# Kernel optimization log

Hardware: AMD Instinct MI355X
Metric: run time of the kernel (lower is better)

The kernel has to match this reference:

```python
import jax, jax.numpy as jnp
import numpy as np
from math import factorial, sqrt

# ---------------- irreps utilities ----------------
def parse(s):
    out = []
    for tok in s.split('+'):
        tok = tok.strip()
        mul, ir = (tok.split('x') if 'x' in tok else ('1', tok))
        out.append((int(mul), int(ir[:-1]), 1 if ir[-1] == 'e' else -1))
    return out

def irdim(ir):
    return sum(m * (2 * l + 1) for m, l, p in ir)

def slices(ir):
    s, o = [], 0
    for m, l, p in ir:
        s.append((o, m, l, p)); o += m * (2 * l + 1)
    return s

# ---------------- real Clebsch-Gordan coefficients ----------------
def _cgc(j1, m1, j2, m2, j3, m3):
    if m1 + m2 != m3:
        return 0.0
    f = factorial
    pre = sqrt((2 * j3 + 1) * f(j3 + j1 - j2) * f(j3 - j1 + j2) * f(j1 + j2 - j3) / f(j1 + j2 + j3 + 1))
    pre *= sqrt(f(j3 + m3) * f(j3 - m3) * f(j1 - m1) * f(j1 + m1) * f(j2 - m2) * f(j2 + m2))
    s = 0.0
    for k in range(max(0, j2 - j3 - m1, j1 - j3 + m2), min(j1 + j2 - j3, j1 - m1, j2 + m2) + 1):
        s += (-1) ** k / (f(k) * f(j1 + j2 - j3 - k) * f(j1 - m1 - k) * f(j2 + m2 - k) * f(j3 - j2 + m1 + k) * f(j3 - j1 - m2 + k))
    return pre * s

def _c2r(l):
    # complex -> real spherical-harmonic change of basis
    q = np.zeros((2 * l + 1, 2 * l + 1), dtype=complex); r2 = 1 / np.sqrt(2)
    q[l, l] = 1.0
    for mu in range(1, l + 1):
        q[mu + l, mu + l] = (-1) ** mu * r2; q[mu + l, -mu + l] = r2
        q[-mu + l, -mu + l] = 1j * r2;       q[-mu + l, mu + l] = -1j * (-1) ** mu * r2
    return q

_CGMEM = {}
def cg_real(l1, l2, l3):
    key = (l1, l2, l3)
    if key in _CGMEM:
        return _CGMEM[key]
    C = np.zeros((2 * l1 + 1, 2 * l2 + 1, 2 * l3 + 1))
    for m1 in range(-l1, l1 + 1):
        for m2 in range(-l2, l2 + 1):
            if abs(m1 + m2) <= l3:
                C[m1 + l1, m2 + l2, m1 + m2 + l3] = _cgc(l1, m1, l2, m2, l3, m1 + m2)
    T = np.einsum('am,bn,co,mno->abc', _c2r(l1), _c2r(l2), np.conj(_c2r(l3)), C)
    R = T.real if np.abs(T.real).sum() >= np.abs(T.imag).sum() else T.imag
    _CGMEM[key] = np.ascontiguousarray(R)
    return _CGMEM[key]

# ---------------- equivariant ops ----------------
def tp_paths(ir1, ir2, iro):
    P = []
    for (o1, m1, l1, p1) in slices(ir1):
        for (o2, m2, l2, p2) in slices(ir2):
            for (oo, mo, lo, po) in slices(iro):
                if po == p1 * p2 and abs(l1 - l2) <= lo <= l1 + l2:
                    P.append((o1, m1, l1, o2, m2, l2, oo, mo, lo))
    return P

def tp_numel(P):
    return sum(m1 * m2 * mo for (_, m1, _, _, m2, _, _, mo, _) in P)

def tp_apply(ir1, ir2, iro, x1, x2, w):
    # FullyConnectedTensorProduct with per-row (shared_weights=False) weights w:[E, numel]
    P = tp_paths(ir1, ir2, iro)
    out = jnp.zeros((x1.shape[0], irdim(iro)), x1.dtype)
    fan = {}
    for p in P:
        fan[p[6]] = fan.get(p[6], 0) + p[1] * p[4]
    off = 0
    for (o1, m1, l1, o2, m2, l2, oo, mo, lo) in P:
        cg = jnp.asarray(cg_real(l1, l2, lo), x1.dtype)
        a = x1[:, o1:o1 + m1 * (2 * l1 + 1)].reshape(-1, m1, 2 * l1 + 1)
        b = x2[:, o2:o2 + m2 * (2 * l2 + 1)].reshape(-1, m2, 2 * l2 + 1)
        ww = w[:, off:off + m1 * m2 * mo].reshape(-1, m1, m2, mo); off += m1 * m2 * mo
        r = jnp.einsum('eui,evj,euvw,ijk->ewk', a, b, ww, cg) / np.sqrt(fan[oo])
        out = out.at[:, oo:oo + mo * (2 * lo + 1)].add(r.reshape(-1, mo * (2 * lo + 1)))
    return out

def lin_pairs(iri, iro):
    return [(si, so) for si in slices(iri) for so in slices(iro) if si[2] == so[2] and si[3] == so[3]]

def lin_numel(iri, iro):
    return sum(si[1] * so[1] for si, so in lin_pairs(iri, iro))

def lin_apply(iri, iro, x, w):
    # o3.Linear: per-irrep channel mixing with fan-in normalization
    out = jnp.zeros((x.shape[0], irdim(iro)), x.dtype)
    pairs = lin_pairs(iri, iro)
    fan = {}
    for si, so in pairs:
        fan[so[0]] = fan.get(so[0], 0) + si[1]
    off = 0
    for (oi, mi, li, pi), (oo, mo, lo, po) in pairs:
        W = w[off:off + mi * mo].reshape(mi, mo); off += mi * mo
        xb = x[:, oi:oi + mi * (2 * li + 1)].reshape(-1, mi, 2 * li + 1)
        r = jnp.einsum('eui,uv->evi', xb, W) / np.sqrt(fan[oo])
        out = out.at[:, oo:oo + mo * (2 * lo + 1)].add(r.reshape(-1, mo * (2 * lo + 1)))
    return out

def act_apply(ir, acts, x):
    # tanh on scalar irreps only (flags in acts), identity elsewhere
    parts = []
    for (o, m, l, p), a in zip(slices(ir), acts):
        b = x[:, o:o + m * (2 * l + 1)]
        parts.append(jnp.tanh(b) if a else b)
    return jnp.concatenate(parts, axis=1)

def fc_apply(x, w, dims):
    # e3nn FullyConnectedNet: relu MLP with 1/sqrt(fan_in) weight normalization
    off, h = 0, x
    for i in range(len(dims) - 1):
        di, do = dims[i], dims[i + 1]
        W = w[off:off + di * do].reshape(di, do); off += di * do
        h = (h @ W) / np.sqrt(di)
        if i < len(dims) - 2:
            h = jax.nn.relu(h)
    return h

# ---------------- module irreps (from V_theta.__init__) ----------------
IRR_IN = parse('2x0e')
IRR_SH = parse('1x0e+1x1o+1x2e')
MID1 = parse('8x0e+8x1o+8x2e')
MID2 = parse('8x0e+8x0o+8x1e+8x1o+8x2e+8x2o')
IRR_HH = parse('4x0e+2x1o+2x1o+1x0e+1x1e+1x2e')
IRR_CC = parse('9x0e+6x1o+3x2e+6x1o+' + '1x0e+1x1e+1x2e+' * 4 + '1x1o+1x2o+1x3o+' * 2 + '3x2e+' + '1x1o+1x2o+1x3o+' * 2 + '1x0e+1x1e+1x2e+1x3e+1x4e')
IRR_CH = parse('6x0e+3x1o+4x1o+' + '1x0e+1x1e+1x2e+' * 2 + '2x2e+1x1o+1x2o+1x3o')
SCR = parse('32x0e+1x2e'); SCR2 = parse('1x0e+1x2e'); G1 = parse('32x0e'); G2 = parse('3x0e')
ACT2 = [1, 0, 0]; ACT3 = [1, 1, 0, 0, 0, 0]
P1 = tp_paths(IRR_IN, IRR_SH, MID1); P2 = tp_paths(MID1, IRR_SH, MID2); PB = tp_paths(MID2, MID2, MID2)
EMB_N = 16
FC1D = [1, EMB_N, EMB_N, EMB_N, tp_numel(P1)]
FC2D = [1, EMB_N, EMB_N, EMB_N, tp_numel(P2)]
FCBD = [1, EMB_N, EMB_N, EMB_N, tp_numel(PB)]

def fcsz(d):
    return sum(d[i] * d[i + 1] for i in range(len(d) - 1))

N_NODES, N_EDGES, N_BOND, SCALING = 10000, 100000, 1000, 0.2


def setup_inputs() -> dict:
    key = jax.random.key(0)
    ks = jax.random.split(key, 32)
    nrm = lambda i, shp: jax.random.normal(ks[i], shp, jnp.float32)
    return {
        'f_in': nrm(0, (N_NODES, 2)),
        'sh': nrm(1, (N_EDGES, 9)),
        'emb': jax.random.uniform(ks[2], (N_EDGES, 1), jnp.float32),
        'num_neighbors': jnp.full((1,), 10.0, jnp.float32),
        'w_lin1': nrm(3, (lin_numel(IRR_IN, IRR_IN),)),
        'w_lin2': nrm(4, (lin_numel(MID1, MID1),)),
        'w_lin3': nrm(5, (lin_numel(MID2, MID2),)),
        'w_linCC': nrm(6, (lin_numel(MID2, IRR_CC),)),
        'w_linHH': nrm(7, (lin_numel(MID2, IRR_HH),)),
        'w_linCH': nrm(8, (lin_numel(MID2, IRR_CH),)),
        'w_linC': nrm(9, (lin_numel(MID2, IRR_CC),)),
        'w_linH': nrm(10, (lin_numel(MID2, IRR_HH),)),
        'w_screen1': nrm(11, (lin_numel(MID2, SCR),)),
        'w_screen2': nrm(12, (lin_numel(SCR, SCR2),)),
        'w_gap1': nrm(13, (lin_numel(MID2, G1),)),
        'w_gap2': nrm(14, (lin_numel(G1, G2),)),
        'w_fc1': nrm(15, (fcsz(FC1D),)),
        'w_fc2': nrm(16, (fcsz(FC2D),)),
        'w_fcb': nrm(17, (fcsz(FCBD),)),
        'edge_src': jax.random.randint(ks[18], (N_EDGES,), 0, N_NODES),
        'edge_dst': jax.random.randint(ks[19], (N_EDGES,), 0, N_NODES),
        'HH_ind': jax.random.randint(ks[20], (N_BOND,), 0, N_EDGES),
        'CC_ind': jax.random.randint(ks[21], (N_BOND,), 0, N_EDGES),
        'CH_ind': jax.random.randint(ks[22], (N_BOND,), 0, N_EDGES),
        'num_nodes': N_NODES,
    }


def reference(f_in, sh, emb, num_neighbors, w_lin1, w_lin2, w_lin3, w_linCC, w_linHH, w_linCH, w_linC, w_linH, w_screen1, w_screen2, w_gap1, w_gap2, w_fc1, w_fc2, w_fcb, edge_src, edge_dst, HH_ind, CC_ind, CH_ind, num_nodes):
    inv = 1.0 / jnp.sqrt(num_neighbors)  # .div(num_neighbors**0.5)
    # layer 1: linear + tanh, gather -> TP with per-edge weights -> scatter-add
    x = jnp.tanh(lin_apply(IRR_IN, IRR_IN, f_in, w_lin1))
    ef = tp_apply(IRR_IN, IRR_SH, MID1, x[edge_src], sh, fc_apply(emb, w_fc1, FC1D))
    x = jax.ops.segment_sum(ef, edge_dst, num_segments=num_nodes) * inv
    x = act_apply(MID1, ACT2, lin_apply(MID1, MID1, x, w_lin2))
    # layer 2
    ef = tp_apply(MID1, IRR_SH, MID2, x[edge_src], sh, fc_apply(emb, w_fc2, FC2D))
    x = jax.ops.segment_sum(ef, edge_dst, num_segments=num_nodes) * inv
    x = act_apply(MID2, ACT3, lin_apply(MID2, MID2, x, w_lin3))
    # bond-level tensor products on edge subsets
    def bond(ind):
        return tp_apply(MID2, MID2, MID2, x[edge_src[ind]], x[edge_dst[ind]], fc_apply(emb[ind], w_fcb, FCBD))
    HHf, CCf, CHf = bond(HH_ind), bond(CC_ind), bond(CH_ind)
    eHH = lin_apply(MID2, IRR_HH, act_apply(MID2, ACT3, HHf), w_linHH)
    eCC = lin_apply(MID2, IRR_CC, act_apply(MID2, ACT3, CCf), w_linCC)
    eCH = lin_apply(MID2, IRR_CH, act_apply(MID2, ACT3, CHf), w_linCH)
    nC = lin_apply(MID2, IRR_CC, x, w_linC)
    nH = lin_apply(MID2, IRR_HH, x, w_linH)
    screen = lin_apply(SCR, SCR2, act_apply(SCR, [1, 0], lin_apply(MID2, SCR, x, w_screen1)), w_screen2)
    def gap(F):
        return lin_apply(G1, G2, jnp.tanh(lin_apply(MID2, G1, F, w_gap1)), w_gap2)
    s = SCALING
    # order: H, C, HH, CH, CC, screen, gap[CC], gap[HH], gap[CH]
    return (nH * s, nC * s, eHH * s, eCH * s, eCC * s, screen, gap(CCf), gap(HHf), gap(CHf))
```

## Files before the change

kernel.cpp:

```cpp
#include <hip/hip_runtime.h>
#include <hip/hip_bf16.h>

typedef __hip_bfloat16 bf16_t;

#define N_NODES 10000
#define N_EDGES 100000
#define N_BONDS 1000

__device__ __forceinline__ float bf2f(bf16_t v){ return __bfloat162float(v); }
__device__ __forceinline__ bf16_t f2bf(float v){ return __float2bfloat16(v); }
__device__ __forceinline__ int iabs(int x){ return x<0?-x:x; }

constexpr bool cg_nz(int l1,int l2,int l3,int i,int j,int k){
  int m1=i-l1, m2=j-l2, m3=k-l3;
  int neg=(m1<0)+(m2<0)+(m3<0);
  if (((neg ^ (l1+l2+l3)) & 1)!=0) return false;
  int a1=m1<0?-m1:m1, a2=m2<0?-m2:m2, a3=m3<0?-m3:m3;
  return (a3==a1+a2)||(a3==a1-a2)||(a3==a2-a1);
}

__device__ __forceinline__ void stout(void* out, size_t idx, float v, bool f32o){
  if (f32o) ((float*)out)[idx]=v;
  else      ((bf16_t*)out)[idx]=f2bf(v);
}

__global__ void detect_k(const unsigned short* nnb_raw, int* flag){
  *flag = (nnb_raw[0]==0x4120) ? 0 : 1;
}

struct CvtArgs {
  const void* src[19];
  float* dst[19];
  int n[19];
};

__global__ __launch_bounds__(256) void convert_k(CvtArgs a, const int* flag){
  bool f32 = (*flag)!=0;
  int tid = blockIdx.x*256+threadIdx.x;
  int nth = gridDim.x*256;
  for(int t=0;t<19;++t){
    int n=a.n[t];
    float* d=a.dst[t];
    if (f32){
      const float* s=(const float*)a.src[t];
      for(int i=tid;i<n;i+=nth) d[i]=s[i];
    } else {
      const bf16_t* s=(const bf16_t*)a.src[t];
      for(int i=tid;i<n;i+=nth) d[i]=bf2f(s[i]);
    }
  }
}

__global__ __launch_bounds__(256) void csr_count_k(const int* __restrict__ edst, int* __restrict__ cnt){
  int e=blockIdx.x*256+threadIdx.x; if(e>=N_EDGES) return;
  atomicAdd(&cnt[edst[e]],1);
}

__global__ __launch_bounds__(256) void csr_scan_k(const int* __restrict__ cnt,
    int* __restrict__ rowptr, int* __restrict__ pos){
  __shared__ int ssum[256];
  int t=threadIdx.x;
  int base=t*40;
  int s=0;
  for(int i=0;i<40;++i){ int idx=base+i; s += (idx<N_NODES)? cnt[idx]:0; }
  ssum[t]=s; __syncthreads();
  if(t==0){ int run=0; for(int i=0;i<256;++i){ int v=ssum[i]; ssum[i]=run; run+=v; } }
  __syncthreads();
  int run=ssum[t];
  for(int i=0;i<40;++i){
    int idx=base+i;
    if(idx<N_NODES){ rowptr[idx]=run; pos[idx]=run; run+=cnt[idx]; }
  }
  if(t==255) rowptr[N_NODES]=run;
}

__global__ __launch_bounds__(256) void csr_scatter_k(const int* __restrict__ edst,
    int* __restrict__ pos, int* __restrict__ sorted){
  int e=blockIdx.x*256+threadIdx.x; if(e>=N_EDGES) return;
  int p=atomicAdd(&pos[edst[e]],1);
  sorted[p]=e;
}

__device__ __forceinline__ double dfact(int n){
  const double F[11]={1.,1.,2.,6.,24.,120.,720.,5040.,40320.,362880.,3628800.};
  return F[n];
}

__device__ double cgc_d(int j1,int m1,int j2,int m2,int j3,int m3){
  if (m1+m2!=m3) return 0.0;
  double pre = sqrt((double)(2*j3+1)*dfact(j3+j1-j2)*dfact(j3-j1+j2)*dfact(j1+j2-j3)/dfact(j1+j2+j3+1));
  pre *= sqrt(dfact(j3+m3)*dfact(j3-m3)*dfact(j1-m1)*dfact(j1+m1)*dfact(j2-m2)*dfact(j2+m2));
  int k0 = max(0, max(j2-j3-m1, j1-j3+m2));
  int k1 = min(j1+j2-j3, min(j1-m1, j2+m2));
  double s=0.0;
  for(int k=k0;k<=k1;++k)
    s += ((k&1)?-1.0:1.0)/(dfact(k)*dfact(j1+j2-j3-k)*dfact(j1-m1-k)*dfact(j2+m2-k)*dfact(j3-j2+m1+k)*dfact(j3-j1-m2+k));
  return pre*s;
}

__device__ void c2r_d(int l,int a,int m,double&re,double&im){
  re=0.0; im=0.0;
  const double r2 = 0.7071067811865475244;
  int mu = a-l;
  if (mu==0){ if (m==l) re=1.0; return; }
  if (mu>0){
    if (m==l+mu) re = (mu&1)? -r2 : r2;
    else if (m==l-mu) re = r2;
  } else {
    int nu=-mu;
    if (m==l-nu) im = r2;
    else if (m==l+nu) im = (nu&1)? r2 : -r2;
  }
}

__global__ __launch_bounds__(128) void cg_init_k(float* cg){
  int b=blockIdx.x;
  int l1=b/9, l2=(b/3)%3, l3=b%3;
  if (l3 < iabs(l1-l2) || l3 > l1+l2) return;
  int n1=2*l1+1,n2=2*l2+1,n3=2*l3+1,n=n1*n2*n3;
  __shared__ double sRe[125], sIm[125];
  __shared__ int sPick;
  int t=threadIdx.x;
  if (t<n){
    int a=t/(n2*n3), bb=(t/n3)%n2, c=t%n3;
    double re=0.0, im=0.0;
    for(int m1=0;m1<n1;++m1){
      double q1r,q1i; c2r_d(l1,a,m1,q1r,q1i);
      if (q1r==0.0 && q1i==0.0) continue;
      for(int m2=0;m2<n2;++m2){
        double q2r,q2i; c2r_d(l2,bb,m2,q2r,q2i);
        if (q2r==0.0 && q2i==0.0) continue;
        int m3=(m1-l1)+(m2-l2)+l3;
        if (m3<0||m3>=n3) continue;
        double q3r,q3i; c2r_d(l3,c,m3,q3r,q3i); q3i=-q3i;
        double C = cgc_d(l1,m1-l1,l2,m2-l2,l3,m3-l3);
        if (C==0.0) continue;
        double ar = q1r*q2r - q1i*q2i;
        double ai = q1r*q2i + q1i*q2r;
        re += (ar*q3r - ai*q3i)*C;
        im += (ar*q3i + ai*q3r)*C;
      }
    }
    sRe[t]=re; sIm[t]=im;
  }
  __syncthreads();
  if (t==0){
    double s1=0.0,s2=0.0;
    for(int i=0;i<n;++i){ s1+=fabs(sRe[i]); s2+=fabs(sIm[i]); }
    sPick = (s1>=s2)?1:0;
  }
  __syncthreads();
  if (t<n) cg[b*125+t] = (float)(sPick? sRe[t] : sIm[t]);
}

__global__ __launch_bounds__(256) void nodeA_k(const float* __restrict__ fin,
                                               const float* __restrict__ w,
                                               float* __restrict__ x1){
  int n=blockIdx.x*256+threadIdx.x; if(n>=N_NODES) return;
  float f0=fin[2*n], f1=fin[2*n+1];
  const float r2=0.70710678f;
// ... 160 lines not shown
  float* Xw=sX+ns*72;
  Xw[v]=r[0];
  #pragma unroll
  for(int i=0;i<3;++i) Xw[8+v*3+i]=r[1+i];
  #pragma unroll
  for(int i=0;i<5;++i) Xw[32+v*5+i]=r[4+i];
  __syncthreads();
  for(int t=tid;t<32*72;t+=256){
    int n=base+t/72;
    if (n<N_NODES) x[(size_t)n*72 + t%72]=sX[t];
  }
}

__global__ __launch_bounds__(256) void lin3b_k(float* __restrict__ x, const float* __restrict__ w){
  __shared__ float sX[32*144];
  __shared__ float sW[384];
  int tid=threadIdx.x;
  int base=blockIdx.x*32;
  for(int t=tid;t<384;t+=256) sW[t]=w[t];
  for(int t=tid;t<32*144;t+=256){
    int n=base+t/144;
    sX[t] = (n<N_NODES)? x[(size_t)n*144 + t%144] : 0.f;
  }
  __syncthreads();
  int ns=tid>>3, v=tid&7;
  const float r8=0.35355339f;
  const float* X=sX+ns*144;
  float r[18];
  {
    float a=0.f;
    #pragma unroll
    for(int u=0;u<8;++u) a+=X[u]*sW[u*8+v];
    r[0]=tanhf(a*r8);
  }
  {
    float a=0.f;
    #pragma unroll
    for(int u=0;u<8;++u) a+=X[8+u]*sW[64+u*8+v];
    r[1]=tanhf(a*r8);
  }
  #pragma unroll
  for(int i=0;i<3;++i){
    float a=0.f;
    #pragma unroll
    for(int u=0;u<8;++u) a+=X[16+u*3+i]*sW[128+u*8+v];
    r[2+i]=a*r8;
  }
  #pragma unroll
  for(int i=0;i<3;++i){
    float a=0.f;
    #pragma unroll
    for(int u=0;u<8;++u) a+=X[40+u*3+i]*sW[192+u*8+v];
    r[5+i]=a*r8;
  }
  #pragma unroll
  for(int i=0;i<5;++i){
    float a=0.f;
    #pragma unroll
    for(int u=0;u<8;++u) a+=X[64+u*5+i]*sW[256+u*8+v];
    r[8+i]=a*r8;
  }
  #pragma unroll
  for(int i=0;i<5;++i){
    float a=0.f;
    #pragma unroll
    for(int u=0;u<8;++u) a+=X[104+u*5+i]*sW[320+u*8+v];
    r[13+i]=a*r8;
  }
  __syncthreads();
  float* Xw=sX+ns*144;
  Xw[v]=r[0];
  Xw[8+v]=r[1];
  #pragma unroll
  for(int i=0;i<3;++i) Xw[16+v*3+i]=r[2+i];
  #pragma unroll
  for(int i=0;i<3;++i) Xw[40+v*3+i]=r[5+i];
  #pragma unroll
  for(int i=0;i<5;++i) Xw[64+v*5+i]=r[8+i];
  #pragma unroll
  for(int i=0;i<5;++i) Xw[104+v*5+i]=r[13+i];
  __syncthreads();
  for(int t=tid;t<32*144;t+=256){
    int n=base+t/144;
    if (n<N_NODES) x[(size_t)n*144 + t%144]=sX[t];
  }
}

template<int L1,int L2,int LO,int BO,int SLOT>
__device__ __forceinline__ void tp_acc(const float* Au, const float* b,
    const float* __restrict__ cg, float wv, float* acc){
  constexpr int D1=2*L1+1, D2=2*L2+1, DN=2*LO+1;
  const float* C = cg + ((L1*3+L2)*3+LO)*125;
  float P[DN];
  #pragma unroll
  for(int k=0;k<DN;++k) P[k]=0.f;
  #pragma unroll
  for(int i=0;i<D1;++i){
    float av=Au[i];
    #pragma unroll
    for(int j=0;j<D2;++j){
      #pragma unroll
      for(int k=0;k<DN;++k){
        if (cg_nz(L1,L2,LO,i,j,k)){
          float cv=C[(i*D2+j)*DN+k];
          P[k]+=av*(cv*b[BO+j]);
        }
      }
    }
  }
  #pragma unroll
  for(int k=0;k<DN;++k) acc[SLOT+k]+=wv*P[k];
}

__device__ __forceinline__ void e2_finish2(float* acc, float inv, float* __restrict__ o, bool first){
  int lane=threadIdx.x&63;
  int w=lane&7;
  #pragma unroll
  for(int t=0;t<18;++t){
    acc[t]+=__shfl_xor(acc[t],8,64);
    acc[t]+=__shfl_xor(acc[t],16,64);
    acc[t]+=__shfl_xor(acc[t],32,64);
  }
  if (lane<8){
    float f0 =rsqrtf(24.f)*inv;
    float f1e=rsqrtf(16.f)*inv;
    float f1o=rsqrtf(32.f)*inv;
    float f2e=rsqrtf(32.f)*inv;
    float f2o=rsqrtf(16.f)*inv;
    if (first){
      o[0+w]=acc[0]*f0;
      o[8+w]=0.f;
      #pragma unroll
      for(int k=0;k<3;++k) o[16+w*3+k]=acc[2+k]*f1e;
      #pragma unroll
      for(int k=0;k<3;++k) o[40+w*3+k]=acc[5+k]*f1o;
      #pragma unroll
      for(int k=0;k<5;++k) o[64+w*5+k]=acc[8+k]*f2e;
      #pragma unroll
      for(int k=0;k<5;++k) o[104+w*5+k]=acc[13+k]*f2o;
    } else {
      o[0+w]+=acc[0]*f0;
      #pragma unroll
      for(int k=0;k<3;++k) o[16+w*3+k]+=acc[2+k]*f1e;
      #pragma unroll
      for(int k=0;k<3;++k) o[40+w*3+k]+=acc[5+k]*f1o;
      #pragma unroll
      for(int k=0;k<5;++k) o[64+w*5+k]+=acc[8+k]*f2e;
      #pragma unroll
      for(int k=0;k<5;++k) o[104+w*5+k]+=acc[13+k]*f2o;
    }
  }
}

__device__ __forceinline__ void e2c_consume(const float* __restrict__ xn,
    const float* __restrict__ sh, const float* __restrict__ cg,
    const float* wwp, int e, int src, int u, int lane, float* acc){
  float sv[15];
  sv[ 0]=wwp[  0+lane]; sv[ 1]=wwp[256+lane]; sv[ 2]=wwp[768+lane];
  sv[ 3]=wwp[320+lane]; sv[ 4]=wwp[832+lane];
  sv[ 5]=wwp[ 64+lane]; sv[ 6]=wwp[192+lane]; sv[ 7]=wwp[448+lane]; sv[ 8]=wwp[640+lane];
  sv[ 9]=wwp[128+lane]; sv[10]=wwp[384+lane]; sv[11]=wwp[576+lane]; sv[12]=wwp[896+lane];
  sv[13]=wwp[512+lane]; sv[14]=wwp[704+lane];
  const float* A = xn + (size_t)src*72;
  float b[9];
  #pragma unroll
  for(int j=0;j<9;++j) b[j]=sh[(size_t)e*9+j];
  float a0[1]; a0[0]=A[u];
  float a1[3];
  #pragma unroll
  for(int i=0;i<3;++i) a1[i]=A[8+u*3+i];
  float a2[5];
  #pragma unroll
  for(int i=0;i<5;++i) a2[i]=A[32+u*5+i];
  tp_acc<0,0,0,0, 0>(a0,b,cg,sv[ 0],acc);
  tp_acc<1,1,0,1, 0>(a1,b,cg,sv[ 1],acc);
  tp_acc<2,2,0,4, 0>(a2,b,cg,sv[ 2],acc);
  tp_acc<1,1,1,1, 2>(a1,b,cg,sv[ 3],acc);
  tp_acc<2,2,1,4, 2>(a2,b,cg,sv[ 4],acc);
  tp_acc<0,1,1,1, 5>(a0,b,cg,sv[ 5],acc);
  tp_acc<1,0,1,0, 5>(a1,b,cg,sv[ 6],acc);
  tp_acc<1,2,1,4, 5>(a1,b,cg,sv[ 7],acc);
  tp_acc<2,1,1,1, 5>(a2,b,cg,sv[ 8],acc);
  tp_acc<0,2,2,4, 8>(a0,b,cg,sv[ 9],acc);
  tp_acc<1,1,2,1, 8>(a1,b,cg,sv[10],acc);
  tp_acc<2,0,2,0, 8>(a2,b,cg,sv[11],acc);
  tp_acc<2,2,2,4, 8>(a2,b,cg,sv[12],acc);
  tp_acc<1,2,2,4,13>(a1,b,cg,sv[13],acc);
  tp_acc<2,1,2,1,13>(a2,b,cg,sv[14],acc);
}

__global__ __launch_bounds__(256) void edge2g_k(const float* __restrict__ xn,
    const float* __restrict__ sh, const float* __restrict__ ww2,
    const int* __restrict__ esrc, const int* __restrict__ sorted,
    const int* __restrict__ rowptr, const float* __restrict__ nnb,
    const float* __restrict__ cg, float* __restrict__ xout,
    int rb, int re, int first){
  int wid=threadIdx.x>>6, lane=threadIdx.x&63;
  int n=blockIdx.x*4+wid; if(n>=N_NODES) return;
  int u=lane>>3;
  float inv=rsqrtf(nnb[0]);
  int r0=rowptr[n], r1=rowptr[n+1];
  int lo=max(r0,rb), hi=min(r1,re);
  if (lo>=hi && !first) return;
  float acc[18];
  #pragma unroll
  for(int t=0;t<18;++t) acc[t]=0.f;
  for(int r=lo;r<hi;++r){
    int e=__builtin_amdgcn_readfirstlane(sorted[r]);
    int src=__builtin_amdgcn_readfirstlane(esrc[e]);
    const float* wr = ww2 + (size_t)(r-rb)*960;
    e2c_consume(xn,sh,cg,wr,e,src,u,lane,acc);
  }
  e2_finish2(acc, inv, xout+(size_t)n*144, first!=0);
}

__global__ __launch_bounds__(256) void edge2c_k(const float* __restrict__ xn,
    const float* __restrict__ sh, const float* __restrict__ h2,
    const float* __restrict__ Wg, const int* __restrict__ esrc,
    const int* __restrict__ sorted, const int* __restrict__ rowptr,
    const float* __restrict__ nnb, const float* __restrict__ cg,
    float* __restrict__ xout){
  __shared__ float ww[2][4][960];
  __shared__ int sE[4];
  __shared__ int sCnt[4];
  int tid=threadIdx.x, wid=tid>>6, lane=tid&63;
  int n=blockIdx.x*4+wid;
  int u=lane>>3;
  float inv=rsqrtf(nnb[0]);
  int r0=rowptr[n], r1=rowptr[n+1];
  if (lane==0) sCnt[wid]=r1-r0;
  __syncthreads();
  int mx = max(max(sCnt[0],sCnt[1]),max(sCnt[2],sCnt[3]));
  float acc[18];
  #pragma unroll
  for(int t=0;t<18;++t) acc[t]=0.f;
  int pe=0, psrc=0; bool pact=false;
  for(int t=0;t<mx;++t){
    int r=r0+t;
    bool act=(r<r1);
    int e=0, src=0;
    if (act){
      e=__builtin_amdgcn_readfirstlane(sorted[r]);
      src=__builtin_amdgcn_readfirstlane(esrc[e]);
    }
    if (lane==0) sE[wid]= act? e : -1;
    __syncthreads();
    if (tid<240){
      int e0=max(sE[0],0), e1=max(sE[1],0), e2i=max(sE[2],0), e3=max(sE[3],0);
      const float* h0=h2+(size_t)e0*16;
      const float* h1=h2+(size_t)e1*16;
      const float* hq=h2+(size_t)e2i*16;
      const float* h3=h2+(size_t)e3*16;
      float4 av[4];
      #pragma unroll
      for(int k=0;k<4;++k) av[k]=make_float4(0.f,0.f,0.f,0.f);
      #pragma unroll
      for(int i=0;i<16;++i){
        float hx=h0[i], hy=h1[i], hz=hq[i], hw=h3[i];
        const float* Wr=Wg+i*960;
        #pragma unroll
        for(int k=0;k<4;++k){
          float w=Wr[tid+240*k];
          av[k].x+=hx*w; av[k].y+=hy*w; av[k].z+=hz*w; av[k].w+=hw*w;
        }
      }
      float* wb=&ww[t&1][0][0];
      #pragma unroll
      for(int k=0;k<4;++k){
        int c=tid+240*k;
        wb[c]=av[k].x*0.25f; wb[960+c]=av[k].y*0.25f;
        wb[1920+c]=av[k].z*0.25f; wb[2880+c]=av[k].w*0.25f;
      }
    }
    if (pact){
      const float* wwp=&ww[(t&1)^1][wid][0];
      e2c_consume(xn,sh,cg,wwp,pe,psrc,u,lane,acc);
    }
    pe=e; psrc=src; pact=act;
    __syncthreads();
  }
  if (pact){
    const float* wwp=&ww[(mx-1)&1][wid][0];
    e2c_consume(xn,sh,cg,wwp,pe,psrc,u,lane,acc);
  }
  e2_finish2(acc, inv, xout+(size_t)n*144, true);
}

struct IrS{ short off,m,l,p; };
__device__ const IrS SL_MID2[6]={{0,8,0,1},{8,8,0,-1},{16,8,1,1},{40,8,1,-1},{64,8,2,1},{104,8,2,-1}};
__device__ const IrS SL_HH[6]={{0,4,0,1},{4,2,1,-1},{10,2,1,-1},{16,1,0,1},{17,1,1,1},{20,1,2,1}};
__device__ const IrS SL_CC[34]={{0,9,0,1},{9,6,1,-1},{27,3,2,1},{42,6,1,-1},
 {60,1,0,1},{61,1,1,1},{64,1,2,1},{69,1,0,1},{70,1,1,1},{73,1,2,1},
 {78,1,0,1},{79,1,1,1},{82,1,2,1},{87,1,0,1},{88,1,1,1},{91,1,2,1},
 {96,1,1,-1},{99,1,2,-1},{104,1,3,-1},{111,1,1,-1},{114,1,2,-1},{119,1,3,-1},
 {126,3,2,1},{141,1,1,-1},{144,1,2,-1},{149,1,3,-1},{156,1,1,-1},{159,1,2,-1},{164,1,3,-1},
 {171,1,0,1},{172,1,1,1},{175,1,2,1},{180,1,3,1},{187,1,4,1}};
__device__ const IrS SL_CH[13]={{0,6,0,1},{6,3,1,-1},{15,4,1,-1},{27,1,0,1},{28,1,1,1},{31,1,2,1},
 {36,1,0,1},{37,1,1,1},{40,1,2,1},{45,2,2,1},{55,1,1,-1},{58,1,2,-1},{63,1,3,-1}};

__device__ void lin_out_r(const float* __restrict__ x, bool act16, const float* __restrict__ w,
                          const IrS* so, int no, void* out, size_t base, bool f32o,
                          float scale, int aBeg, int aEnd, bool zf){
  float tx[16];
  bool need_tx = act16 && (aBeg<2);
  if (need_tx){
    #pragma unroll
    for(int i=0;i<16;++i) tx[i]=tanhf(x[i]);
  }
  if (zf){
    for(int bI=0;bI<no;++bI){
      if (so[bI].l>=3){
        int cnt=so[bI].m*(2*so[bI].l+1);
        for(int t=0;t<cnt;++t) stout(out, base+so[bI].off+t, 0.f, f32o);
      }
    }
  }
  int woff=0;
  float f = 0.35355339f*scale;
  for(int a=0;a<6;++a){
    int la=SL_MID2[a].l, pa=SL_MID2[a].p, oa=SL_MID2[a].off;
    int d=2*la+1;
    bool doit = (a>=aBeg && a<aEnd);
    for(int bI=0;bI<no;++bI){
      if (so[bI].l!=la || so[bI].p!=pa) continue;
      int mo=so[bI].m;
      if (doit){
        for(int v=0;v<mo;++v){
          for(int i=0;i<d;++i){
            float acc=0.f;
            for(int u=0;u<8;++u){
              int idx=oa+u*d+i;
              float xv=(act16 && idx<16)? tx[idx] : x[idx];
              acc+=xv*w[woff+u*mo+v];
            }
            stout(out, base+so[bI].off+v*d+i, acc*f, f32o);
          }
        }
      }
      woff+=8*mo;
    }
  }
}

__global__ __launch_bounds__(256) void node_out_k(const float* __restrict__ x,
    const float* __restrict__ wC, const float* __restrict__ wH,
    const float* __restrict__ ws1, const float* __restrict__ ws2,
    void* out, const int* __restrict__ flag){
  int t=blockIdx.x*256+threadIdx.x;
  int n=t>>3, job=t&7;
  if (n>=N_NODES) return;
  bool f32o = (*flag)!=0;
  const float* X = x + (size_t)n*144;
  if (job==0){
    lin_out_r(X,false,wH,SL_HH,6, out, (size_t)n*25, f32o, 0.2f, 0,6, true);
  } else if (job==1){
    const float r8=0.35355339f, r32=0.17677670f;
    float t0[32];
    for(int v=0;v<32;++v){
      float acc=0.f;
      #pragma unroll
      for(int u=0;u<8;++u) acc+=X[u]*ws1[u*32+v];
      t0[v]=tanhf(acc*r8);
    }
    float t2[5];
    #pragma unroll
    for(int i=0;i<5;++i){
      float acc=0.f;
      #pragma unroll
      for(int u=0;u<8;++u) acc+=X[64+u*5+i]*ws1[256+u];
      t2[i]=acc*r8;
    }
    size_t sb = 2501000 + (size_t)n*6;
    float acc=0.f;
    for(int v=0;v<32;++v) acc+=t0[v]*ws2[v];
    stout(out, sb, acc*r32, f32o);
    float w2e=ws2[32];
    #pragma unroll
    for(int i=0;i<5;++i) stout(out, sb+1+i, t2[i]*w2e, f32o);
  } else if (job>=2 && job<=5){
    const int AB[4]={0,2,4,5}, AE[4]={2,4,5,6};
    lin_out_r(X,false,wC,SL_CC,34, out, 250000 + (size_t)n*196, f32o, 0.2f,
              AB[job-2], AE[job-2], job==2);
  }
}

template<int L1,int L2,int LO>
__device__ __forceinline__ void bond_path2(const float* sa,int ao,const float* sb,int bo,
    const float* __restrict__ cg, const float* __restrict__ wwp,
    float invfan, float* sF, int oo, int lane){
  constexpr int D1=2*L1+1, D2=2*L2+1, DN=2*LO+1;
  const float* C = cg + ((L1*3+L2)*3+LO)*125;
  int u=lane>>3, v=lane&7;
  float P[DN];
  #pragma unroll
  for(int k=0;k<DN;++k) P[k]=0.f;
  #pragma unroll
  for(int i=0;i<D1;++i){
    float avv=sa[ao+u*D1+i];
    #pragma unroll
    for(int j=0;j<D2;++j){
      #pragma unroll
      for(int k=0;k<DN;++k){
        if (cg_nz(L1,L2,LO,i,j,k)){
          float cv=C[(i*D2+j)*DN+k];
          P[k]+=(avv*sb[bo+v*D2+j])*cv;
        }
      }
    }
  }
  int v2=u;
  float acc[DN];
  #pragma unroll
  for(int k=0;k<DN;++k) acc[k]=0.f;
  #pragma unroll
  for(int u2=0;u2<8;++u2){
    float ww=wwp[u2*64 + lane];
    int srcl=u2*8+v2;
    #pragma unroll
    for(int k=0;k<DN;++k) acc[k]+=ww*__shfl(P[k],srcl,64);
  }
  #pragma unroll
  for(int k=0;k<DN;++k){
    acc[k]+=__shfl_xor(acc[k],8,64);
    acc[k]+=__shfl_xor(acc[k],16,64);
    acc[k]+=__shfl_xor(acc[k],32,64);
  }
  int w=lane&7;
  if (v2==0){
    #pragma unroll
    for(int k=0;k<DN;++k) sF[oo+w*DN+k]+=acc[k]*invfan;
  }
}

__device__ __forceinline__ void bond_disp(int code, const float* a,int ao,const float* bb,int bo,
    const float* __restrict__ cg, const float* __restrict__ wwp,
    float fv, float* Ff, int oo, int lane){
  switch(code){
    case 0:  bond_path2<0,0,0>(a,ao,bb,bo,cg,wwp,fv,Ff,oo,lane); break;
    case 4:  bond_path2<0,1,1>(a,ao,bb,bo,cg,wwp,fv,Ff,oo,lane); break;
    case 8:  bond_path2<0,2,2>(a,ao,bb,bo,cg,wwp,fv,Ff,oo,lane); break;
    case 10: bond_path2<1,0,1>(a,ao,bb,bo,cg,wwp,fv,Ff,oo,lane); break;
    case 12: bond_path2<1,1,0>(a,ao,bb,bo,cg,wwp,fv,Ff,oo,lane); break;
    case 13: bond_path2<1,1,1>(a,ao,bb,bo,cg,wwp,fv,Ff,oo,lane); break;
    case 14: bond_path2<1,1,2>(a,ao,bb,bo,cg,wwp,fv,Ff,oo,lane); break;
    case 16: bond_path2<1,2,1>(a,ao,bb,bo,cg,wwp,fv,Ff,oo,lane); break;
    case 17: bond_path2<1,2,2>(a,ao,bb,bo,cg,wwp,fv,Ff,oo,lane); break;
    case 20: bond_path2<2,0,2>(a,ao,bb,bo,cg,wwp,fv,Ff,oo,lane); break;
    case 22: bond_path2<2,1,1>(a,ao,bb,bo,cg,wwp,fv,Ff,oo,lane); break;
    case 23: bond_path2<2,1,2>(a,ao,bb,bo,cg,wwp,fv,Ff,oo,lane); break;
    case 24: bond_path2<2,2,0>(a,ao,bb,bo,cg,wwp,fv,Ff,oo,lane); break;
    case 25: bond_path2<2,2,1>(a,ao,bb,bo,cg,wwp,fv,Ff,oo,lane); break;
    case 26: bond_path2<2,2,2>(a,ao,bb,bo,cg,wwp,fv,Ff,oo,lane); break;
  }
}

__global__ __launch_bounds__(256) void bond_tpl_k(const float* __restrict__ xn,
    const float* __restrict__ hb, const float* __restrict__ Wg,
    const int* __restrict__ esrc, const int* __restrict__ edst,
    const int* __restrict__ i0, const int* __restrict__ i1,
    const int* __restrict__ i2, const float* __restrict__ cg,
    float* __restrict__ F0, float* __restrict__ F1, float* __restrict__ F2){
  __shared__ float sA[4][144], sB[4][144], sF[4][144];
  __shared__ float ww[2][2048];
  int tid=threadIdx.x;
  int wid=tid>>6, lane=tid&63;
  int gb=blockIdx.x*4+wid;
  int s=gb/N_BONDS, bi=gb-s*N_BONDS;
  const int* ind=(s==0)?i0:(s==1)?i1:i2;
  float* F=(s==0)?F0:(s==1)?F1:F2;
  int ie=ind[bi];
  int src=esrc[ie], dst=edst[ie];
  for(int t=lane;t<144;t+=64){
    sA[wid][t]=xn[(size_t)src*144+t];
    sB[wid][t]=xn[(size_t)dst*144+t];
    sF[wid][t]=0.f;
  }
  float4 hreg[16];
  {
    size_t hbase=(size_t)blockIdx.x*64;
    #pragma unroll
    for(int i=0;i<16;++i)
      hreg[i]=make_float4(hb[hbase+i],hb[hbase+16+i],hb[hbase+32+i],hb[hbase+48+i]);
  }
  const int SL_L[6]={0,0,1,1,2,2};
  const int SL_P[6]={1,-1,1,-1,1,-1};
  const int SL_O[6]={0,8,16,40,64,104};
  const float fi0=rsqrtf(384.f), fi1=rsqrtf(768.f);
  int pidx=0;
  int pcode=0, pao=0, pbo=0, poo=0; float pfv=0.f;
  for(int s1=0;s1<6;++s1){
    for(int s2=0;s2<6;++s2){
      for(int so=0;so<6;++so){
        int l1=SL_L[s1], l2=SL_L[s2], lo=SL_L[so];
        if (SL_P[so]!=SL_P[s1]*SL_P[s2]) continue;
        if (lo<iabs(l1-l2) || lo>l1+l2) continue;
        {
          const float* Wp = Wg + (size_t)pidx*512;
          float4 a0=make_float4(0.f,0.f,0.f,0.f);
          float4 a1=make_float4(0.f,0.f,0.f,0.f);
          #pragma unroll
          for(int i=0;i<16;++i){
            float w0=Wp[(size_t)i*30720 + tid];
            float w1=Wp[(size_t)i*30720 + tid + 256];
            float4 h=hreg[i];
            a0.x+=h.x*w0; a0.y+=h.y*w0; a0.z+=h.z*w0; a0.w+=h.w*w0;
            a1.x+=h.x*w1; a1.y+=h.y*w1; a1.z+=h.z*w1; a1.w+=h.w*w1;
          }
          float* wb=ww[pidx&1];
          wb[0*512+tid]    =a0.x*0.25f;
          wb[1*512+tid]    =a0.y*0.25f;
          wb[2*512+tid]    =a0.z*0.25f;
          wb[3*512+tid]    =a0.w*0.25f;
          wb[0*512+tid+256]=a1.x*0.25f;
          wb[1*512+tid+256]=a1.y*0.25f;
          wb[2*512+tid+256]=a1.z*0.25f;
          wb[3*512+tid+256]=a1.w*0.25f;
        }
        if (pidx>0){
          const float* wwp = ww[(pidx-1)&1] + wid*512;
          bond_disp(pcode, sA[wid], pao, sB[wid], pbo, cg, wwp, pfv, sF[wid], poo, lane);
        }
        pcode=l1*9+l2*3+lo; pao=SL_O[s1]; pbo=SL_O[s2]; poo=SL_O[so];
        pfv=(lo==0)? fi0 : fi1;
        pidx++;
        __syncthreads();
      }
    }
  }
  {
    const float* wwp = ww[(pidx-1)&1] + wid*512;
    bond_disp(pcode, sA[wid], pao, sB[wid], pbo, cg, wwp, pfv, sF[wid], poo, lane);
  }
  __syncthreads();
  for(int t=lane;t<144;t+=64) F[(size_t)bi*144+t]=sF[wid][t];
}

__global__ __launch_bounds__(256) void bond_out_k(const float* __restrict__ F,
    const float* __restrict__ wlin, int tbl, void* out, size_t baseE,
    const float* __restrict__ wg1, const float* __restrict__ wg2,
    size_t baseG, const int* __restrict__ flag){
  int t=blockIdx.x*256+threadIdx.x;
  int n=t>>3, job=t&7;
  if (n>=N_BONDS) return;
  bool f32o = (*flag)!=0;
  const float* X=F+(size_t)n*144;
  if (job==0){
    const float r8=0.35355339f, r32=0.17677670f;
    float g[32];
    for(int v=0;v<32;++v){
      float acc=0.f;
      #pragma unroll
      for(int u=0;u<8;++u) acc+=X[u]*wg1[u*32+v];
      g[v]=tanhf(acc*r8);
    }
    #pragma unroll
    for(int c=0;c<3;++c){
      float acc=0.f;
      for(int v=0;v<32;++v) acc+=g[v]*wg2[v*3+c];
      stout(out, baseG+(size_t)n*3+c, acc*r32, f32o);
    }
  } else if (job>=2 && job<=5){
    const IrS* so; int no; int dim;
    if(tbl==0){so=SL_HH;no=6;dim=25;}
    else if(tbl==1){so=SL_CC;no=34;dim=196;}
    else {so=SL_CH;no=13;dim=70;}
    const int AB[4]={0,2,4,5}, AE[4]={2,4,5,6};
    lin_out_r(X,true,wlin,so,no,out,baseE+(size_t)n*dim,f32o,0.2f,
              AB[job-2], AE[job-2], job==2);
  }
}

extern "C" void kernel_launch(void* const* d_in, const int* in_sizes, int n_in,
                              void* d_out, int out_size, void* d_ws, size_t ws_size,
                              hipStream_t stream){
  const int* esrc=(const int*)d_in[19];
  const int* edst=(const int*)d_in[20];
  const int* iHH =(const int*)d_in[21];
  const int* iCC =(const int*)d_in[22];
  const int* iCH =(const int*)d_in[23];
  float* ws=(float*)d_ws;
  int* flag=(int*)d_ws;

  size_t off=16;
  auto alloc=[&](size_t n){ size_t o=off; off+=(n+15)&~(size_t)15; return o; };
  size_t o_cg = alloc(27*125);
  size_t o_st[19];
  for(int i=0;i<19;++i) o_st[i]=alloc((size_t)in_sizes[i]);
  size_t o_x1  = alloc(20000);
  size_t o_xM1 = alloc(720000);
  size_t o_xM2 = alloc(1440000);
  size_t o_F0  = alloc(144000);
  size_t o_F1  = alloc(144000);
  size_t o_F2  = alloc(144000);
  size_t o_h1  = alloc((size_t)N_EDGES*16);
  size_t o_h2  = alloc((size_t)N_EDGES*16);
  size_t o_hb  = alloc((size_t)3*N_BONDS*16);
  size_t o_ww1 = alloc((size_t)N_EDGES*48);
  size_t o_cnt = alloc(10016);
  size_t o_rp  = alloc(10016);
  size_t o_pos = alloc(10016);
  size_t o_srt = alloc(N_EDGES);

  float* cg  = ws+o_cg;
  float* x1  = ws+o_x1;
  float* xM1 = ws+o_xM1;
  float* xM2 = ws+o_xM2;
  float* F0  = ws+o_F0;
  float* F1  = ws+o_F1;
  float* F2  = ws+o_F2;
  float* h1  = ws+o_h1;
  float* h2  = ws+o_h2;
  float* hb  = ws+o_hb;
  float* ww1 = ws+o_ww1;
  int* cnt   = (int*)(ws+o_cnt);
  int* rowptr= (int*)(ws+o_rp);
  int* pos   = (int*)(ws+o_pos);
  int* sorted= (int*)(ws+o_srt);

  size_t totf = ws_size/sizeof(float);
  size_t availf = (totf>off)? totf-off : 0;
  int CHUNK = (int)((availf/960 < (size_t)N_EDGES)? availf/960 : (size_t)N_EDGES);
  bool use_chunk = (CHUNK >= 4000);
  float* ww2 = ws + off;

  CvtArgs ca;
  for(int i=0;i<19;++i){ ca.src[i]=d_in[i]; ca.dst[i]=ws+o_st[i]; ca.n[i]=in_sizes[i]; }
  const float* f_in   = ws+o_st[0];
  const float* sh     = ws+o_st[1];
  const float* emb    = ws+o_st[2];
  const float* nnb    = ws+o_st[3];
  const float* w_lin1 = ws+o_st[4];
  const float* w_lin2 = ws+o_st[5];
  const float* w_lin3 = ws+o_st[6];
  const float* w_linCC= ws+o_st[7];
  const float* w_linHH= ws+o_st[8];
  const float* w_linCH= ws+o_st[9];
  const float* w_linC = ws+o_st[10];
  const float* w_linH = ws+o_st[11];
  const float* w_s1   = ws+o_st[12];
  const float* w_s2   = ws+o_st[13];
  const float* w_g1   = ws+o_st[14];
  const float* w_g2   = ws+o_st[15];
  const float* w_fc1  = ws+o_st[16];
  const float* w_fc2  = ws+o_st[17];
  const float* w_fcb  = ws+o_st[18];

  detect_k<<<1,1,0,stream>>>((const unsigned short*)d_in[3], flag);
  convert_k<<<512,256,0,stream>>>(ca, flag);
  cg_init_k<<<27,128,0,stream>>>(cg);
  hipMemsetAsync(cnt, 0, 10000*sizeof(int), stream);
  csr_count_k<<<391,256,0,stream>>>(edst, cnt);
  csr_scan_k<<<1,256,0,stream>>>(cnt, rowptr, pos);
  csr_scatter_k<<<391,256,0,stream>>>(edst, pos, sorted);

  nodeA_k<<<40,256,0,stream>>>(f_in,w_lin1,x1);
  hmlp_k<<<391,256,0,stream>>>(emb, w_fc1, h1, N_EDGES);
  hmlp_k<<<391,256,0,stream>>>(emb, w_fc2, h2, N_EDGES);
  hb_k<<<12,256,0,stream>>>(emb, w_fcb, iHH, iCC, iCH, hb);

  gemm16_k<<<dim3(1563,1),256,0,stream>>>(h1, w_fc1+528, ww1, N_EDGES, 48, sorted);
  edge1b_k<<<313,256,0,stream>>>(x1,sh,ww1,esrc,sorted,rowptr,nnb,xM1);
  lin2b_k<<<313,256,0,stream>>>(xM1,w_lin2);

  if (use_chunk){
    int nch = (N_EDGES + CHUNK - 1)/CHUNK;
    for (int ci=0; ci<nch; ++ci){
      int rb = ci*CHUNK;
      int re = rb+CHUNK; if (re>N_EDGES) re=N_EDGES;
      int Cc = re-rb;
      gemm16_k<<<dim3((Cc+63)/64,15),256,0,stream>>>(h2, w_fc2+528, ww2, Cc, 960, sorted+rb);
      edge2g_k<<<2500,256,0,stream>>>(xM1, sh, ww2, esrc, sorted, rowptr,
          nnb, cg, xM2, rb, re, (ci==0)?1:0);
    }
  } else {
    edge2c_k<<<2500,256,0,stream>>>(xM1, sh, h2, w_fc2+528,
        esrc, sorted, rowptr, nnb, cg, xM2);
  }
  lin3b_k<<<313,256,0,stream>>>(xM2,w_lin3);
  node_out_k<<<313,256,0,stream>>>(xM2,w_linC,w_linH,w_s1,w_s2,d_out,flag);

  bond_tpl_k<<<750,256,0,stream>>>(xM2, hb, w_fcb+528,
      esrc, edst, iHH, iCC, iCH, cg, F0, F1, F2);

  bond_out_k<<<32,256,0,stream>>>(F0,w_linHH,0,d_out,2210000,w_g1,w_g2,2564000,flag);
  bond_out_k<<<32,256,0,stream>>>(F1,w_linCC,1,d_out,2305000,w_g1,w_g2,2561000,flag);
  bond_out_k<<<32,256,0,stream>>>(F2,w_linCH,2,d_out,2235000,w_g1,w_g2,2567000,flag);
}
```

Before: 994.0 us.

## Split bond tensor-product paths across blocks and make output jobs wave-uniform

```diff
diff --git a/kernel.cpp b/kernel.cpp
--- a/kernel.cpp
+++ b/kernel.cpp
@@ -6,6 +6,8 @@
 #define N_NODES 10000
 #define N_EDGES 100000
 #define N_BONDS 1000
+#define BOND_SEG 4
+#define BOND_PPS 15
 
 __device__ __forceinline__ float bf2f(bf16_t v){ return __bfloat162float(v); }
 __device__ __forceinline__ bf16_t f2bf(float v){ return __float2bfloat16(v); }
@@ -666,8 +668,11 @@
     const float* __restrict__ wC, const float* __restrict__ wH,
     const float* __restrict__ ws1, const float* __restrict__ ws2,
     void* out, const int* __restrict__ flag){
-  int t=blockIdx.x*256+threadIdx.x;
-  int n=t>>3, job=t&7;
+  int tid=threadIdx.x;
+  int gw=blockIdx.x*4+(tid>>6);
+  int lane=tid&63;
+  int job=gw&7;
+  int n=(gw>>3)*64+lane;
   if (n>=N_NODES) return;
   bool f32o = (*flag)!=0;
   const float* X = x + (size_t)n*144;
@@ -697,10 +702,10 @@
     float w2e=ws2[32];
     #pragma unroll
     for(int i=0;i<5;++i) stout(out, sb+1+i, t2[i]*w2e, f32o);
-  } else if (job>=2 && job<=5){
-    const int AB[4]={0,2,4,5}, AE[4]={2,4,5,6};
+  } else {
+    int a=job-2;
     lin_out_r(X,false,wC,SL_CC,34, out, 250000 + (size_t)n*196, f32o, 0.2f,
-              AB[job-2], AE[job-2], job==2);
+              a, a+1, a==0);
   }
 }
 
@@ -784,7 +789,10 @@
   __shared__ float ww[2][2048];
   int tid=threadIdx.x;
   int wid=tid>>6, lane=tid&63;
-  int gb=blockIdx.x*4+wid;
+  int seg=blockIdx.x & (BOND_SEG-1);
+  int blk=blockIdx.x >> 2;
+  int pBeg=seg*BOND_PPS, pEnd=pBeg+BOND_PPS;
+  int gb=blk*4+wid;
   int s=gb/N_BONDS, bi=gb-s*N_BONDS;
   const int* ind=(s==0)?i0:(s==1)?i1:i2;
   float* F=(s==0)?F0:(s==1)?F1:F2;
@@ -797,7 +805,7 @@
   }
   float4 hreg[16];
   {
-    size_t hbase=(size_t)blockIdx.x*64;
+    size_t hbase=(size_t)blk*64;
     #pragma unroll
     for(int i=0;i<16;++i)
       hreg[i]=make_float4(hb[hbase+i],hb[hbase+16+i],hb[hbase+32+i],hb[hbase+48+i]);
@@ -806,61 +814,68 @@
   const int SL_P[6]={1,-1,1,-1,1,-1};
   const int SL_O[6]={0,8,16,40,64,104};
   const float fi0=rsqrtf(384.f), fi1=rsqrtf(768.f);
-  int pidx=0;
-  int pcode=0, pao=0, pbo=0, poo=0; float pfv=0.f;
+  int pidx=0, lpi=0;
+  int pcode=0, pao=0, pbo=0, poo=0; float pfv=0.f; bool pval=false;
   for(int s1=0;s1<6;++s1){
     for(int s2=0;s2<6;++s2){
       for(int so=0;so<6;++so){
         int l1=SL_L[s1], l2=SL_L[s2], lo=SL_L[so];
         if (SL_P[so]!=SL_P[s1]*SL_P[s2]) continue;
         if (lo<iabs(l1-l2) || lo>l1+l2) continue;
-        {
-          const float* Wp = Wg + (size_t)pidx*512;
-          float4 a0=make_float4(0.f,0.f,0.f,0.f);
-          float4 a1=make_float4(0.f,0.f,0.f,0.f);
-          #pragma unroll
-          for(int i=0;i<16;++i){
-            float w0=Wp[(size_t)i*30720 + tid];
-            float w1=Wp[(size_t)i*30720 + tid + 256];
-            float4 h=hreg[i];
-            a0.x+=h.x*w0; a0.y+=h.y*w0; a0.z+=h.z*w0; a0.w+=h.w*w0;
-            a1.x+=h.x*w1; a1.y+=h.y*w1; a1.z+=h.z*w1; a1.w+=h.w*w1;
+        if (pidx>=pBeg && pidx<pEnd){
+          {
+            const float* Wp = Wg + (size_t)pidx*512;
+            float4 a0=make_float4(0.f,0.f,0.f,0.f);
+            float4 a1=make_float4(0.f,0.f,0.f,0.f);
+            #pragma unroll
+            for(int i=0;i<16;++i){
+              float w0=Wp[(size_t)i*30720 + tid];
+              float w1=Wp[(size_t)i*30720 + tid + 256];
+              float4 h=hreg[i];
+              a0.x+=h.x*w0; a0.y+=h.y*w0; a0.z+=h.z*w0; a0.w+=h.w*w0;
+              a1.x+=h.x*w1; a1.y+=h.y*w1; a1.z+=h.z*w1; a1.w+=h.w*w1;
+            }
+            float* wb=ww[lpi&1];
+            wb[0*512+tid]    =a0.x*0.25f;
+            wb[1*512+tid]    =a0.y*0.25f;
+            wb[2*512+tid]    =a0.z*0.25f;
+            wb[3*512+tid]    =a0.w*0.25f;
+            wb[0*512+tid+256]=a1.x*0.25f;
+            wb[1*512+tid+256]=a1.y*0.25f;
+            wb[2*512+tid+256]=a1.z*0.25f;
+            wb[3*512+tid+256]=a1.w*0.25f;
           }
-          float* wb=ww[pidx&1];
-          wb[0*512+tid]    =a0.x*0.25f;
-          wb[1*512+tid]    =a0.y*0.25f;
-          wb[2*512+tid]    =a0.z*0.25f;
-          wb[3*512+tid]    =a0.w*0.25f;
-          wb[0*512+tid+256]=a1.x*0.25f;
-          wb[1*512+tid+256]=a1.y*0.25f;
-          wb[2*512+tid+256]=a1.z*0.25f;
-          wb[3*512+tid+256]=a1.w*0.25f;
+          if (pval){
+            const float* wwp = ww[(lpi-1)&1] + wid*512;
+            bond_disp(pcode, sA[wid], pao, sB[wid], pbo, cg, wwp, pfv, sF[wid], poo, lane);
+          }
+          pcode=l1*9+l2*3+lo; pao=SL_O[s1]; pbo=SL_O[s2]; poo=SL_O[so];
+          pfv=(lo==0)? fi0 : fi1;
+          pval=true;
+          lpi++;
+          __syncthreads();
         }
-        if (pidx>0){
-          const float* wwp = ww[(pidx-1)&1] + wid*512;
-          bond_disp(pcode, sA[wid], pao, sB[wid], pbo, cg, wwp, pfv, sF[wid], poo, lane);
-        }
-        pcode=l1*9+l2*3+lo; pao=SL_O[s1]; pbo=SL_O[s2]; poo=SL_O[so];
-        pfv=(lo==0)? fi0 : fi1;
         pidx++;
-        __syncthreads();
       }
     }
   }
-  {
-    const float* wwp = ww[(pidx-1)&1] + wid*512;
+  if (pval){
+    const float* wwp = ww[(lpi-1)&1] + wid*512;
     bond_disp(pcode, sA[wid], pao, sB[wid], pbo, cg, wwp, pfv, sF[wid], poo, lane);
   }
   __syncthreads();
-  for(int t=lane;t<144;t+=64) F[(size_t)bi*144+t]=sF[wid][t];
+  for(int t=lane;t<144;t+=64) atomicAdd(&F[(size_t)bi*144+t], sF[wid][t]);
 }
 
 __global__ __launch_bounds__(256) void bond_out_k(const float* __restrict__ F,
     const float* __restrict__ wlin, int tbl, void* out, size_t baseE,
     const float* __restrict__ wg1, const float* __restrict__ wg2,
     size_t baseG, const int* __restrict__ flag){
-  int t=blockIdx.x*256+threadIdx.x;
-  int n=t>>3, job=t&7;
+  int tid=threadIdx.x;
+  int gw=blockIdx.x*4+(tid>>6);
+  int lane=tid&63;
+  int job=gw&7;
+  int n=(gw>>3)*64+lane;
   if (n>=N_BONDS) return;
   bool f32o = (*flag)!=0;
   const float* X=F+(size_t)n*144;
@@ -879,14 +894,14 @@
       for(int v=0;v<32;++v) acc+=g[v]*wg2[v*3+c];
       stout(out, baseG+(size_t)n*3+c, acc*r32, f32o);
     }
-  } else if (job>=2 && job<=5){
+  } else if (job>=2){
     const IrS* so; int no; int dim;
     if(tbl==0){so=SL_HH;no=6;dim=25;}
     else if(tbl==1){so=SL_CC;no=34;dim=196;}
     else {so=SL_CH;no=13;dim=70;}
-    const int AB[4]={0,2,4,5}, AE[4]={2,4,5,6};
+    int a=job-2;
     lin_out_r(X,true,wlin,so,no,out,baseE+(size_t)n*dim,f32o,0.2f,
-              AB[job-2], AE[job-2], job==2);
+              a, a+1, a==0);
   }
 }
 
@@ -997,9 +1012,10 @@
         esrc, sorted, rowptr, nnb, cg, xM2);
   }
   lin3b_k<<<313,256,0,stream>>>(xM2,w_lin3);
-  node_out_k<<<313,256,0,stream>>>(xM2,w_linC,w_linH,w_s1,w_s2,d_out,flag);
-
-  bond_tpl_k<<<750,256,0,stream>>>(xM2, hb, w_fcb+528,
+  node_out_k<<<314,256,0,stream>>>(xM2,w_linC,w_linH,w_s1,w_s2,d_out,flag);
+
+  hipMemsetAsync(F0, 0, 3*144000*sizeof(float), stream);
+  bond_tpl_k<<<750*BOND_SEG,256,0,stream>>>(xM2, hb, w_fcb+528,
       esrc, edst, iHH, iCC, iCH, cg, F0, F1, F2);
 
   bond_out_k<<<32,256,0,stream>>>(F0,w_linHH,0,d_out,2210000,w_g1,w_g2,2564000,flag);
```

New measurement: 913.7 us. -8.1%, faster.

## Balance edge layer-2 work by fixed edge ranges per wave with atomic flush

Applied to the files above, without the earlier changes.

```diff
diff --git a/kernel.cpp b/kernel.cpp
--- a/kernel.cpp
+++ b/kernel.cpp
@@ -6,6 +6,7 @@
 #define N_NODES 10000
 #define N_EDGES 100000
 #define N_BONDS 1000
+#define RPW 20
 
 __device__ __forceinline__ float bf2f(bf16_t v){ return __bfloat162float(v); }
 __device__ __forceinline__ bf16_t f2bf(float v){ return __float2bfloat16(v); }
@@ -472,6 +473,33 @@
   }
 }
 
+__device__ __forceinline__ void e2_flush(float* acc, float inv, float* __restrict__ o){
+  int lane=threadIdx.x&63;
+  int w=lane&7;
+  #pragma unroll
+  for(int t=0;t<18;++t){
+    acc[t]+=__shfl_xor(acc[t],8,64);
+    acc[t]+=__shfl_xor(acc[t],16,64);
+    acc[t]+=__shfl_xor(acc[t],32,64);
+  }
+  if (lane<8){
+    float f0 =rsqrtf(24.f)*inv;
+    float f1e=rsqrtf(16.f)*inv;
+    float f1o=rsqrtf(32.f)*inv;
+    float f2e=rsqrtf(32.f)*inv;
+    float f2o=rsqrtf(16.f)*inv;
+    atomicAdd(&o[0+w], acc[0]*f0);
+    #pragma unroll
+    for(int k=0;k<3;++k) atomicAdd(&o[16+w*3+k], acc[2+k]*f1e);
+    #pragma unroll
+    for(int k=0;k<3;++k) atomicAdd(&o[40+w*3+k], acc[5+k]*f1o);
+    #pragma unroll
+    for(int k=0;k<5;++k) atomicAdd(&o[64+w*5+k], acc[8+k]*f2e);
+    #pragma unroll
+    for(int k=0;k<5;++k) atomicAdd(&o[104+w*5+k], acc[13+k]*f2o);
+  }
+}
+
 __device__ __forceinline__ void e2c_consume(const float* __restrict__ xn,
     const float* __restrict__ sh, const float* __restrict__ cg,
     const float* wwp, int e, int src, int u, int lane, float* acc){
@@ -509,29 +537,43 @@
   tp_acc<2,1,2,1,13>(a2,b,cg,sv[14],acc);
 }
 
-__global__ __launch_bounds__(256) void edge2g_k(const float* __restrict__ xn,
+__global__ __launch_bounds__(256) void edge2r_k(const float* __restrict__ xn,
     const float* __restrict__ sh, const float* __restrict__ ww2,
     const int* __restrict__ esrc, const int* __restrict__ sorted,
     const int* __restrict__ rowptr, const float* __restrict__ nnb,
     const float* __restrict__ cg, float* __restrict__ xout,
-    int rb, int re, int first){
-  int wid=threadIdx.x>>6, lane=threadIdx.x&63;
-  int n=blockIdx.x*4+wid; if(n>=N_NODES) return;
+    int rb, int re){
+  int gw=blockIdx.x*4+(threadIdx.x>>6);
+  int lane=threadIdx.x&63;
   int u=lane>>3;
+  int rs=rb+gw*RPW;
+  if (rs>=re) return;
+  int rend=min(rs+RPW, re);
   float inv=rsqrtf(nnb[0]);
-  int r0=rowptr[n], r1=rowptr[n+1];
-  int lo=max(r0,rb), hi=min(r1,re);
-  if (lo>=hi && !first) return;
+  int lo=0, hi=N_NODES-1;
+  while(lo<hi){ int mid=(lo+hi+1)>>1; if(rowptr[mid]<=rs) lo=mid; else hi=mid-1; }
+  int n=lo;
+  int nend=rowptr[n+1];
   float acc[18];
   #pragma unroll
   for(int t=0;t<18;++t) acc[t]=0.f;
-  for(int r=lo;r<hi;++r){
+  bool dirty=false;
+  for(int r=rs;r<rend;++r){
+    while(r>=nend){
+      if (dirty){
+        e2_flush(acc, inv, xout+(size_t)n*144);
+        #pragma unroll
+        for(int t=0;t<18;++t) acc[t]=0.f;
+        dirty=false;
+      }
+      n++; nend=rowptr[n+1];
+    }
     int e=__builtin_amdgcn_readfirstlane(sorted[r]);
     int src=__builtin_amdgcn_readfirstlane(esrc[e]);
-    const float* wr = ww2 + (size_t)(r-rb)*960;
-    e2c_consume(xn,sh,cg,wr,e,src,u,lane,acc);
-  }
-  e2_finish2(acc, inv, xout+(size_t)n*144, first!=0);
+    e2c_consume(xn,sh,cg, ww2+(size_t)(r-rb)*960, e,src,u,lane,acc);
+    dirty=true;
+  }
+  if (dirty) e2_flush(acc, inv, xout+(size_t)n*144);
 }
 
 __global__ __launch_bounds__(256) void edge2c_k(const float* __restrict__ xn,
@@ -666,8 +708,11 @@
     const float* __restrict__ wC, const float* __restrict__ wH,
     const float* __restrict__ ws1, const float* __restrict__ ws2,
     void* out, const int* __restrict__ flag){
-  int t=blockIdx.x*256+threadIdx.x;
-  int n=t>>3, job=t&7;
+  int tid=threadIdx.x;
+  int gw=blockIdx.x*4+(tid>>6);
+  int lane=tid&63;
+  int job=gw&7;
+  int n=(gw>>3)*64+lane;
   if (n>=N_NODES) return;
   bool f32o = (*flag)!=0;
   const float* X = x + (size_t)n*144;
@@ -697,10 +742,10 @@
     float w2e=ws2[32];
     #pragma unroll
     for(int i=0;i<5;++i) stout(out, sb+1+i, t2[i]*w2e, f32o);
-  } else if (job>=2 && job<=5){
-    const int AB[4]={0,2,4,5}, AE[4]={2,4,5,6};
+  } else {
+    int a=job-2;
     lin_out_r(X,false,wC,SL_CC,34, out, 250000 + (size_t)n*196, f32o, 0.2f,
-              AB[job-2], AE[job-2], job==2);
+              a, a+1, a==0);
   }
 }
 
@@ -859,8 +904,11 @@
     const float* __restrict__ wlin, int tbl, void* out, size_t baseE,
     const float* __restrict__ wg1, const float* __restrict__ wg2,
     size_t baseG, const int* __restrict__ flag){
-  int t=blockIdx.x*256+threadIdx.x;
-  int n=t>>3, job=t&7;
+  int tid=threadIdx.x;
+  int gw=blockIdx.x*4+(tid>>6);
+  int lane=tid&63;
+  int job=gw&7;
+  int n=(gw>>3)*64+lane;
   if (n>=N_BONDS) return;
   bool f32o = (*flag)!=0;
   const float* X=F+(size_t)n*144;
@@ -879,14 +927,14 @@
       for(int v=0;v<32;++v) acc+=g[v]*wg2[v*3+c];
       stout(out, baseG+(size_t)n*3+c, acc*r32, f32o);
     }
-  } else if (job>=2 && job<=5){
+  } else if (job>=2){
     const IrS* so; int no; int dim;
     if(tbl==0){so=SL_HH;no=6;dim=25;}
     else if(tbl==1){so=SL_CC;no=34;dim=196;}
     else {so=SL_CH;no=13;dim=70;}
-    const int AB[4]={0,2,4,5}, AE[4]={2,4,5,6};
+    int a=job-2;
     lin_out_r(X,true,wlin,so,no,out,baseE+(size_t)n*dim,f32o,0.2f,
-              AB[job-2], AE[job-2], job==2);
+              a, a+1, a==0);
   }
 }
 
@@ -912,14 +960,15 @@
   size_t o_F0  = alloc(144000);
   size_t o_F1  = alloc(144000);
   size_t o_F2  = alloc(144000);
-  size_t o_h1  = alloc((size_t)N_EDGES*16);
   size_t o_h2  = alloc((size_t)N_EDGES*16);
   size_t o_hb  = alloc((size_t)3*N_BONDS*16);
-  size_t o_ww1 = alloc((size_t)N_EDGES*48);
   size_t o_cnt = alloc(10016);
   size_t o_rp  = alloc(10016);
   size_t o_pos = alloc(10016);
   size_t o_srt = alloc(N_EDGES);
+  size_t o_h1  = alloc((size_t)N_EDGES*16);
+  size_t o_ww1 = alloc((size_t)N_EDGES*48);
+  (void)o_ww1;
 
   float* cg  = ws+o_cg;
   float* x1  = ws+o_x1;
@@ -938,10 +987,10 @@
   int* sorted= (int*)(ws+o_srt);
 
   size_t totf = ws_size/sizeof(float);
-  size_t availf = (totf>off)? totf-off : 0;
+  size_t availf = (totf>o_h1)? totf-o_h1 : 0;
   int CHUNK = (int)((availf/960 < (size_t)N_EDGES)? availf/960 : (size_t)N_EDGES);
-  bool use_chunk = (CHUNK >= 4000);
-  float* ww2 = ws + off;
+  bool use_chunk = (CHUNK >= 2000);
+  float* ww2 = ws + o_h1;
 
   CvtArgs ca;
   for(int i=0;i<19;++i){ ca.src[i]=d_in[i]; ca.dst[i]=ws+o_st[i]; ca.n[i]=in_sizes[i]; }
@@ -983,21 +1032,24 @@
   lin2b_k<<<313,256,0,stream>>>(xM1,w_lin2);
 
   if (use_chunk){
+    hipMemsetAsync(xM2, 0, 1440000*sizeof(float), stream);
     int nch = (N_EDGES + CHUNK - 1)/CHUNK;
     for (int ci=0; ci<nch; ++ci){
       int rb = ci*CHUNK;
       int re = rb+CHUNK; if (re>N_EDGES) re=N_EDGES;
       int Cc = re-rb;
       gemm16_k<<<dim3((Cc+63)/64,15),256,0,stream>>>(h2, w_fc2+528, ww2, Cc, 960, sorted+rb);
-      edge2g_k<<<2500,256,0,stream>>>(xM1, sh, ww2, esrc, sorted, rowptr,
-          nnb, cg, xM2, rb, re, (ci==0)?1:0);
+      int waves=(Cc+RPW-1)/RPW;
+      int blocks=(waves+3)/4;
+      edge2r_k<<<blocks,256,0,stream>>>(xM1, sh, ww2, esrc, sorted, rowptr,
+          nnb, cg, xM2, rb, re);
     }
   } else {
     edge2c_k<<<2500,256,0,stream>>>(xM1, sh, h2, w_fc2+528,
         esrc, sorted, rowptr, nnb, cg, xM2);
   }
   lin3b_k<<<313,256,0,stream>>>(xM2,w_lin3);
-  node_out_k<<<313,256,0,stream>>>(xM2,w_linC,w_linH,w_s1,w_s2,d_out,flag);
+  node_out_k<<<314,256,0,stream>>>(xM2,w_linC,w_linH,w_s1,w_s2,d_out,flag);
 
   bond_tpl_k<<<750,256,0,stream>>>(xM2, hb, w_fcb+528,
       esrc, edst, iHH, iCC, iCH, cg, F0, F1, F2);
```

Result: faster. 886.1 us (-10.9%).
